# Kernel tuning notes

Measured on AMD Instinct MI355X. Metric: run time of the kernel, lower is better.

Reference implementation:

```python
import jax, jax.numpy as jnp
import numpy as np

N_NODES = 100000
N_EDGES = 1600000
D_FEAT = 128


def setup_inputs() -> dict:
    key = jax.random.key(0)
    k1, k2, k3 = jax.random.split(key, 3)
    feat = jax.random.normal(k1, (N_NODES, D_FEAT), dtype=jnp.float32)
    src = jax.random.randint(k2, (N_EDGES,), 0, N_NODES, dtype=jnp.int32)
    dst = jax.random.randint(k3, (N_EDGES,), 0, N_NODES, dtype=jnp.int32)
    return {"feat": feat, "src": src, "dst": dst}


def reference(feat, src, dst):
    n = feat.shape[0]
    ones = jnp.ones(src.shape[0], dtype=feat.dtype)
    # out-degree of each node (as message source), clamped to >= 1
    deg_o = jnp.clip(jax.ops.segment_sum(ones, src, num_segments=n), 1.0)
    norm_l = deg_o ** -0.5  # [N]
    feat_scaled = feat * norm_l[:, None]
    # copy_u + sum aggregation: gather from src, scatter-add to dst
    agg = jax.ops.segment_sum(feat_scaled[src], dst, num_segments=n)
    # in-degree normalization on destination side
    deg_i = jnp.clip(jax.ops.segment_sum(ones, dst, num_segments=n), 1.0)
    norm_r = deg_i ** -0.5
    return agg * norm_r[:, None]
```

## Files before the change

kernel.cpp:

```cpp
#include <hip/hip_runtime.h>
#include <hip/hip_fp16.h>

#define D_FEAT      128
#define S_BIN       256
#define BUCKET_BITS 7
#define BUCKET_SZ   128
#define NB_MAX      1024
#define SORT_CAP    6144
#define BIGB        1024
#define CAP         2432
#define CAPB        2432

typedef float f32x4 __attribute__((ext_vector_type(4)));

__global__ __launch_bounds__(BIGB) void scatter_direct_kernel(
        const int* __restrict__ src, const int* __restrict__ dst,
        int* __restrict__ fillD, int* __restrict__ fillS,
        int* __restrict__ colp, unsigned char* __restrict__ colp_src,
        int n_edges, int nb, int slice_len) {
    __shared__ int hd[NB_MAX];
    __shared__ int hs[NB_MAX];
    int s = blockIdx.x, tid = threadIdx.x;
    for (int i = tid; i < nb; i += BIGB) { hd[i] = 0; hs[i] = 0; }
    __syncthreads();
    int beg = s * slice_len;
    int end = beg + slice_len; if (end > n_edges) end = n_edges;
    for (int i = beg + tid; i < end; i += BIGB) {
        atomicAdd(&hd[dst[i] >> BUCKET_BITS], 1);
        atomicAdd(&hs[src[i] >> BUCKET_BITS], 1);
    }
    __syncthreads();
    for (int b = tid; b < nb; b += BIGB) {
        int c  = hd[b];
        hd[b] = b * CAP  + atomicAdd(&fillD[b], c);
        int c2 = hs[b];
        hs[b] = b * CAPB + atomicAdd(&fillS[b], c2);
    }
    __syncthreads();
    for (int i = beg + tid; i < end; i += BIGB) {
        int d = dst[i], sv = src[i];
        int p = atomicAdd(&hd[d >> BUCKET_BITS], 1);
        colp[p] = sv | ((d & (BUCKET_SZ - 1)) << 20);
        int q = atomicAdd(&hs[sv >> BUCKET_BITS], 1);
        colp_src[q] = (unsigned char)(sv & (BUCKET_SZ - 1));
    }
}

__global__ __launch_bounds__(512) void sortconv_kernel(
        int* __restrict__ colp, const unsigned char* __restrict__ colp_src,
        const int* __restrict__ fillD, const int* __restrict__ fillS,
        int* __restrict__ node_off, const float* __restrict__ feat,
        __half* __restrict__ feat16, int n_nodes, int nb) {
    __shared__ int buf[SORT_CAP];
    __shared__ int cnt[BUCKET_SZ];
    __shared__ int sa[BUCKET_SZ];
    __shared__ int sb[BUCKET_SZ];
    __shared__ float snl[BUCKET_SZ];
    int tid = threadIdx.x;
    const int NT = 512;

    if ((int)blockIdx.x >= nb) {
        int b = blockIdx.x - nb;
        int begS = b * CAPB;
        int mS = fillS[b];
        if (tid < BUCKET_SZ) cnt[tid] = 0;
        __syncthreads();
        for (int i = tid; i < mS; i += NT)
            atomicAdd(&cnt[colp_src[begS + i]], 1);
        __syncthreads();
        int node0 = b << BUCKET_BITS;
        int bn = n_nodes - node0; if (bn > BUCKET_SZ) bn = BUCKET_SZ;
        if (tid < BUCKET_SZ) {
            int c = cnt[tid]; if (c < 1) c = 1;
            snl[tid] = rsqrtf((float)c);
        }
        __syncthreads();
        int total = bn * (D_FEAT / 8);
        for (int i = tid; i < total; i += NT) {
            int row = i >> 4, q = i & 15;
            float nl = snl[row];
            const f32x4* fp = (const f32x4*)(feat + (size_t)(node0 + row) * D_FEAT) + q * 2;
            f32x4 a = __builtin_nontemporal_load(fp);
            f32x4 bv = __builtin_nontemporal_load(fp + 1);
            __half2 h0 = __floats2half2_rn(a.x * nl, a.y * nl);
            __half2 h1 = __floats2half2_rn(a.z * nl, a.w * nl);
            __half2 h2 = __floats2half2_rn(bv.x * nl, bv.y * nl);
            __half2 h3 = __floats2half2_rn(bv.z * nl, bv.w * nl);
            uint4 o;
            o.x = *(unsigned int*)&h0; o.y = *(unsigned int*)&h1;
            o.z = *(unsigned int*)&h2; o.w = *(unsigned int*)&h3;
            ((uint4*)(feat16 + (size_t)(node0 + row) * D_FEAT))[q] = o;
        }
        return;
    }

    int b = blockIdx.x;
    int beg = b * CAP;
    int m = fillD[b]; if (m > SORT_CAP) m = SORT_CAP;
    if (tid < BUCKET_SZ) cnt[tid] = 0;
    __syncthreads();
    for (int i = tid; i < m; i += NT) {
        int v = colp[beg + i];
        buf[i] = v;
        atomicAdd(&cnt[(v >> 20) & (BUCKET_SZ - 1)], 1);
    }
    __syncthreads();
    int* rp = sa; int* wp = sb;
    if (tid < BUCKET_SZ) sa[tid] = cnt[tid];
    __syncthreads();
    for (int d = 1; d < BUCKET_SZ; d <<= 1) {
        if (tid < BUCKET_SZ) wp[tid] = rp[tid] + (tid >= d ? rp[tid - d] : 0);
        __syncthreads();
        int* t = rp; rp = wp; wp = t;
    }
    int node0 = b << BUCKET_BITS;
    int bn = n_nodes - node0; if (bn > BUCKET_SZ) bn = BUCKET_SZ;
    if (tid < BUCKET_SZ) {
        int ex = rp[tid] - cnt[tid];
        wp[tid] = ex;
        if (tid < bn)
            node_off[node0 + tid] = (cnt[tid] << 22) | (beg + ex);
    }
    __syncthreads();
    for (int i = tid; i < m; i += NT) {
        int v = buf[i];
        int p = atomicAdd(&wp[(v >> 20) & (BUCKET_SZ - 1)], 1);
        colp[beg + p] = v & 0xFFFFF;
    }
    for (int i = m + tid; i < CAP; i += NT)
        colp[beg + i] = 0;
}

__global__ __launch_bounds__(256) void pull_csr_kernel(
        const __half* __restrict__ feat16, const int* __restrict__ col,
        const int* __restrict__ node_off, float* __restrict__ out,
        int n_nodes, int colp_len) {
    int lane = threadIdx.x & 63;
    int wid  = (int)(((long long)blockIdx.x * blockDim.x + threadIdx.x) >> 6);
    int h  = lane >> 5;
    int g  = (lane >> 4) & 1;
    int dl = lane & 15;
    int node = wid * 2 + h;
    bool nvalid = node < n_nodes;
    int nsafe = nvalid ? node : n_nodes - 1;
    int pk = node_off[nsafe];
    int s = pk & 0x3FFFFF;
    int m = nvalid ? (pk >> 22) : 0;
    int om = __shfl_xor(m, 32, 64);
    int mm = m > om ? m : om;

    float a0=0.f,a1=0.f,a2=0.f,a3=0.f,a4=0.f,a5=0.f,a6=0.f,a7=0.f;
    const uint4* rowb = (const uint4*)feat16;

    for (int base = 0; base < mm; base += 32) {
        int remh = m - base;
        int ci = lane & 31;
        if (ci >= remh) ci = (remh > 0) ? remh - 1 : 0;
        int cidx = s + base + ci;
        if (cidx >= colp_len) cidx = colp_len - 1;
        int cv = col[cidx];
        int lim = mm - base; if (lim > 32) lim = 32;
        for (int k = 0; k < lim; k += 2) {
            int srcl = (lane & 32) + k + g;
            int idx = __shfl(cv, srcl, 64);
            uint4 hv = rowb[((size_t)(unsigned)idx << 4) + dl];
            float wm = (base + k + g < m) ? 1.f : 0.f;
            float2 f;
            f = __half22float2(*(__half2*)&hv.x); a0 += wm * f.x; a1 += wm * f.y;
            f = __half22float2(*(__half2*)&hv.y); a2 += wm * f.x; a3 += wm * f.y;
            f = __half22float2(*(__half2*)&hv.z); a4 += wm * f.x; a5 += wm * f.y;
            f = __half22float2(*(__half2*)&hv.w); a6 += wm * f.x; a7 += wm * f.y;
        }
    }

    a0 += __shfl_xor(a0, 16, 64); a1 += __shfl_xor(a1, 16, 64);
    a2 += __shfl_xor(a2, 16, 64); a3 += __shfl_xor(a3, 16, 64);
    a4 += __shfl_xor(a4, 16, 64); a5 += __shfl_xor(a5, 16, 64);
    a6 += __shfl_xor(a6, 16, 64); a7 += __shfl_xor(a7, 16, 64);

    if (nvalid && g == 0) {
        int c = m < 1 ? 1 : m;
        float nr = rsqrtf((float)c);
        f32x4 o0 = {a0 * nr, a1 * nr, a2 * nr, a3 * nr};
        f32x4 o1 = {a4 * nr, a5 * nr, a6 * nr, a7 * nr};
        f32x4* op = (f32x4*)(out + (size_t)node * D_FEAT) + dl * 2;
        __builtin_nontemporal_store(o0, op);
        __builtin_nontemporal_store(o1, op + 1);
    }
}

extern "C" void kernel_launch(void* const* d_in, const int* in_sizes, int n_in,
                              void* d_out, int out_size, void* d_ws, size_t ws_size,
                              hipStream_t stream) {
    const float* feat = (const float*)d_in[0];
    const int*   src  = (const int*)d_in[1];
    const int*   dst  = (const int*)d_in[2];
    float* out = (float*)d_out;

    int n_nodes = in_sizes[0] / D_FEAT;
    int n_edges = in_sizes[1];
    int nb = (n_nodes + BUCKET_SZ - 1) / BUCKET_SZ;
    int sl = (n_edges + S_BIN - 1) / S_BIN;
    int colp_len = nb * CAP;

    auto alignup = [](size_t x) { return (x + 255) & ~(size_t)255; };
    char* p = (char*)d_ws;
    int*    node_off = (int*)p;            p += alignup((size_t)n_nodes * 4);
    int*    fills    = (int*)p;            p += alignup((size_t)2 * nb * 4);
    int*    fillD    = fills;
    int*    fillS    = fills + nb;
    int*    colp     = (int*)p;            p += alignup(((size_t)colp_len + 4096) * 4);
    unsigned char* colp_src = (unsigned char*)p; p += alignup((size_t)nb * CAPB + 4096);
    __half* feat16   = (__half*)p;

    hipMemsetAsync(fills, 0, (size_t)2 * nb * sizeof(int), stream);

    scatter_direct_kernel<<<S_BIN, BIGB, 0, stream>>>(src, dst, fillD, fillS, colp, colp_src,
                                                      n_edges, nb, sl);

    sortconv_kernel<<<2 * nb, 512, 0, stream>>>(colp, colp_src, fillD, fillS, node_off,
                                                feat, feat16, n_nodes, nb);

    {
        long long waves = ((long long)n_nodes + 1) / 2;
        long long total = waves * 64;
        pull_csr_kernel<<<(int)((total + 255) / 256), 256, 0, stream>>>(feat16, colp, node_off,
                                                                        out, n_nodes, colp_len);
    }
}
```

Baseline: 212.7 us.

## Move fp16 feature conversion into scatter kernel and apply source norm in gather

The fp32-to-fp16 conversion of features moves out of the sort kernel and into the tail of the scatter kernel, where it runs without the out-degree scale. The sort kernel now only writes a per-node norm_l array, and the pull kernel loads norm_l[src] for each edge and folds it into the accumulation weight. The aim is to shorten the sort kernel and overlap the conversion traffic with the scatter phase. The cost is one extra scattered 4-byte load per edge in the gather kernel and a longer scatter kernel.

```diff
diff --git a/kernel.cpp b/kernel.cpp
--- a/kernel.cpp
+++ b/kernel.cpp
@@ -13,11 +13,12 @@
 
 typedef float f32x4 __attribute__((ext_vector_type(4)));
 
-__global__ __launch_bounds__(BIGB) void scatter_direct_kernel(
+__global__ __launch_bounds__(BIGB) void scatterconv_kernel(
         const int* __restrict__ src, const int* __restrict__ dst,
         int* __restrict__ fillD, int* __restrict__ fillS,
         int* __restrict__ colp, unsigned char* __restrict__ colp_src,
-        int n_edges, int nb, int slice_len) {
+        const float* __restrict__ feat, __half* __restrict__ feat16,
+        int n_edges, int nb, int slice_len, int total16, int conv_per_blk) {
     __shared__ int hd[NB_MAX];
     __shared__ int hs[NB_MAX];
     int s = blockIdx.x, tid = threadIdx.x;
@@ -44,18 +45,32 @@
         int q = atomicAdd(&hs[sv >> BUCKET_BITS], 1);
         colp_src[q] = (unsigned char)(sv & (BUCKET_SZ - 1));
     }
-}
-
-__global__ __launch_bounds__(512) void sortconv_kernel(
+    int cbeg = s * conv_per_blk;
+    int cend = cbeg + conv_per_blk; if (cend > total16) cend = total16;
+    for (int t = cbeg + tid; t < cend; t += BIGB) {
+        const f32x4* fp = (const f32x4*)feat + (size_t)t * 2;
+        f32x4 a = __builtin_nontemporal_load(fp);
+        f32x4 bv = __builtin_nontemporal_load(fp + 1);
+        __half2 h0 = __floats2half2_rn(a.x, a.y);
+        __half2 h1 = __floats2half2_rn(a.z, a.w);
+        __half2 h2 = __floats2half2_rn(bv.x, bv.y);
+        __half2 h3 = __floats2half2_rn(bv.z, bv.w);
+        uint4 o;
+        o.x = *(unsigned int*)&h0; o.y = *(unsigned int*)&h1;
+        o.z = *(unsigned int*)&h2; o.w = *(unsigned int*)&h3;
+        ((uint4*)feat16)[t] = o;
+    }
+}
+
+__global__ __launch_bounds__(512) void sortcount_kernel(
         int* __restrict__ colp, const unsigned char* __restrict__ colp_src,
         const int* __restrict__ fillD, const int* __restrict__ fillS,
-        int* __restrict__ node_off, const float* __restrict__ feat,
-        __half* __restrict__ feat16, int n_nodes, int nb) {
+        int* __restrict__ node_off, float* __restrict__ norm_l,
+        int n_nodes, int nb) {
     __shared__ int buf[SORT_CAP];
     __shared__ int cnt[BUCKET_SZ];
     __shared__ int sa[BUCKET_SZ];
     __shared__ int sb[BUCKET_SZ];
-    __shared__ float snl[BUCKET_SZ];
     int tid = threadIdx.x;
     const int NT = 512;
 
@@ -70,26 +85,9 @@
         __syncthreads();
         int node0 = b << BUCKET_BITS;
         int bn = n_nodes - node0; if (bn > BUCKET_SZ) bn = BUCKET_SZ;
-        if (tid < BUCKET_SZ) {
+        if (tid < bn) {
             int c = cnt[tid]; if (c < 1) c = 1;
-            snl[tid] = rsqrtf((float)c);
-        }
-        __syncthreads();
-        int total = bn * (D_FEAT / 8);
-        for (int i = tid; i < total; i += NT) {
-            int row = i >> 4, q = i & 15;
-            float nl = snl[row];
-            const f32x4* fp = (const f32x4*)(feat + (size_t)(node0 + row) * D_FEAT) + q * 2;
-            f32x4 a = __builtin_nontemporal_load(fp);
-            f32x4 bv = __builtin_nontemporal_load(fp + 1);
-            __half2 h0 = __floats2half2_rn(a.x * nl, a.y * nl);
-            __half2 h1 = __floats2half2_rn(a.z * nl, a.w * nl);
-            __half2 h2 = __floats2half2_rn(bv.x * nl, bv.y * nl);
-            __half2 h3 = __floats2half2_rn(bv.z * nl, bv.w * nl);
-            uint4 o;
-            o.x = *(unsigned int*)&h0; o.y = *(unsigned int*)&h1;
-            o.z = *(unsigned int*)&h2; o.w = *(unsigned int*)&h3;
-            ((uint4*)(feat16 + (size_t)(node0 + row) * D_FEAT))[q] = o;
+            norm_l[node0 + tid] = rsqrtf((float)c);
         }
         return;
     }
@@ -133,8 +131,8 @@
 
 __global__ __launch_bounds__(256) void pull_csr_kernel(
         const __half* __restrict__ feat16, const int* __restrict__ col,
-        const int* __restrict__ node_off, float* __restrict__ out,
-        int n_nodes, int colp_len) {
+        const int* __restrict__ node_off, const float* __restrict__ norm_l,
+        float* __restrict__ out, int n_nodes, int colp_len) {
     int lane = threadIdx.x & 63;
     int wid  = (int)(((long long)blockIdx.x * blockDim.x + threadIdx.x) >> 6);
     int h  = lane >> 5;
@@ -163,8 +161,9 @@
         for (int k = 0; k < lim; k += 2) {
             int srcl = (lane & 32) + k + g;
             int idx = __shfl(cv, srcl, 64);
+            float nl = norm_l[idx];
             uint4 hv = rowb[((size_t)(unsigned)idx << 4) + dl];
-            float wm = (base + k + g < m) ? 1.f : 0.f;
+            float wm = (base + k + g < m) ? nl : 0.f;
             float2 f;
             f = __half22float2(*(__half2*)&hv.x); a0 += wm * f.x; a1 += wm * f.y;
             f = __half22float2(*(__half2*)&hv.y); a2 += wm * f.x; a3 += wm * f.y;
@@ -202,10 +201,13 @@
     int nb = (n_nodes + BUCKET_SZ - 1) / BUCKET_SZ;
     int sl = (n_edges + S_BIN - 1) / S_BIN;
     int colp_len = nb * CAP;
+    int total16 = n_nodes * (D_FEAT / 8);
+    int conv_per_blk = (total16 + S_BIN - 1) / S_BIN;
 
     auto alignup = [](size_t x) { return (x + 255) & ~(size_t)255; };
     char* p = (char*)d_ws;
     int*    node_off = (int*)p;            p += alignup((size_t)n_nodes * 4);
+    float*  norm_l   = (float*)p;          p += alignup((size_t)n_nodes * 4);
     int*    fills    = (int*)p;            p += alignup((size_t)2 * nb * 4);
     int*    fillD    = fills;
     int*    fillS    = fills + nb;
@@ -215,16 +217,18 @@
 
     hipMemsetAsync(fills, 0, (size_t)2 * nb * sizeof(int), stream);
 
-    scatter_direct_kernel<<<S_BIN, BIGB, 0, stream>>>(src, dst, fillD, fillS, colp, colp_src,
-                                                      n_edges, nb, sl);
-
-    sortconv_kernel<<<2 * nb, 512, 0, stream>>>(colp, colp_src, fillD, fillS, node_off,
-                                                feat, feat16, n_nodes, nb);
+    scatterconv_kernel<<<S_BIN, BIGB, 0, stream>>>(src, dst, fillD, fillS, colp, colp_src,
+                                                   feat, feat16, n_edges, nb, sl,
+                                                   total16, conv_per_blk);
+
+    sortcount_kernel<<<2 * nb, 512, 0, stream>>>(colp, colp_src, fillD, fillS, node_off,
+                                                 norm_l, n_nodes, nb);
 
     {
         long long waves = ((long long)n_nodes + 1) / 2;
         long long total = waves * 64;
         pull_csr_kernel<<<(int)((total + 255) / 256), 256, 0, stream>>>(feat16, colp, node_off,
-                                                                        out, n_nodes, colp_len);
-    }
-}
+                                                                        norm_l, out, n_nodes,
+                                                                        colp_len);
+    }
+}
```

New measurement: 222.7 us. +4.7%, slower.
